# Kernel optimization log

Hardware: AMD Instinct MI355X
Metric: run time of the kernel (lower is better)

Reference implementation:

```python
import jax, jax.numpy as jnp
import numpy as np

B, T, F, H, O = 64, 4096, 100, 200, 1


def setup_inputs() -> dict:
    key = jax.random.key(0)
    ks = jax.random.split(key, 7)
    s_i = 1.0 / np.sqrt(F)
    s_h = 1.0 / np.sqrt(H)
    return {
        "x": jax.random.normal(ks[0], (B, T, F), dtype=jnp.float32),
        # input-to-hidden weights for gates [r, z, n], concatenated: [F, 3H]
        "Wi": jax.random.uniform(ks[1], (F, 3 * H), jnp.float32, -s_i, s_i),
        "bi": jnp.zeros((3 * H,), jnp.float32),
        # hidden-to-hidden weights for gates [r, z, n]: [H, 3H] (no bias for r,z in flax GRUCell)
        "Wh": jax.random.uniform(ks[2], (H, 3 * H), jnp.float32, -s_h, s_h),
        "bhn": jnp.zeros((H,), jnp.float32),  # bias only on the h->n projection
        "Wo": jax.random.uniform(ks[3], (H, O), jnp.float32, -s_h, s_h),
        "bo": jnp.zeros((O,), jnp.float32),
    }


def _gru_forward(x, Wi, bi, Wh, bhn):
    # Precompute input projections for all timesteps: [B, T, 3H]
    gi_all = jnp.einsum("btf,fg->btg", x, Wi) + bi
    gi_all = jnp.transpose(gi_all, (1, 0, 2))  # [T, B, 3H]
    h0 = jnp.zeros((x.shape[0], Wh.shape[0]), x.dtype)

    def step(h, gi):
        hh = h @ Wh  # [B, 3H]
        r = jax.nn.sigmoid(gi[:, :H] + hh[:, :H])
        z = jax.nn.sigmoid(gi[:, H:2 * H] + hh[:, H:2 * H])
        n = jnp.tanh(gi[:, 2 * H:] + r * (hh[:, 2 * H:] + bhn))
        h_new = (1.0 - z) * n + z * h  # flax GRUCell convention
        return h_new, h_new

    _, hs = jax.lax.scan(step, h0, gi_all)  # hs: [T, B, H]
    return jnp.transpose(hs, (1, 0, 2))  # [B, T, H]


def reference(x, Wi, bi, Wh, bhn, Wo, bo):
    hs = _gru_forward(x, Wi, bi, Wh, bhn)
    return jnp.einsum("bth,ho->bto", hs, Wo) + bo  # [B, T, O]
```

## Files before the change

kernel.cpp:

```cpp
#include <hip/hip_runtime.h>
#include <cstdint>

#define B_  64
#define T_  4096
#define F_  100
#define H_  200
#define G_  600

typedef _Float16 half2_t __attribute__((ext_vector_type(2)));

__device__ __forceinline__ float sigmoidf_(float x) {
    return 1.0f / (1.0f + __expf(-x));
}
__device__ __forceinline__ float tanh_fast_(float x) {
    float e = __expf(-2.0f * x);
    return (1.0f - e) / (1.0f + e);
}

__device__ __forceinline__ float fdot2_(half2_t a, half2_t b, float c) {
#if __has_builtin(__builtin_amdgcn_fdot2)
    return __builtin_amdgcn_fdot2(a, b, c, false);
#else
    return fmaf((float)a.x, (float)b.x, fmaf((float)a.y, (float)b.y, c));
#endif
}

__device__ __forceinline__ float dpp_xor1_add(float x) {
    int xi = __float_as_int(x);
    int yi = __builtin_amdgcn_update_dpp(0, xi, 0xB1, 0xF, 0xF, true);
    return x + __int_as_float(yi);
}

__global__ void prep_whp(const float* __restrict__ Wh, half2_t* __restrict__ whp) {
    int i = blockIdx.x * 256 + threadIdx.x;
    if (i < 104 * G_) {
        int k = i / G_, c = i - k * G_;
        half2_t v;
        v.x = (k < 100) ? (_Float16)Wh[(2 * k) * G_ + c] : (_Float16)0.f;
        v.y = (k < 100) ? (_Float16)Wh[(2 * k + 1) * G_ + c] : (_Float16)0.f;
        whp[i] = v;
    }
}

__global__ __launch_bounds__(640, 1)
void gi_kernel(const float* __restrict__ x, const float* __restrict__ Wi,
               const float* __restrict__ bi, float* __restrict__ gi,
               int t0, int TC) {
    __shared__ float xT[F_ * 68];
    int row0 = blockIdx.x * 64;
    int b    = row0 / TC;
    int tc0  = row0 - b * TC;
    const float* xrow = x + ((size_t)b * T_ + t0 + tc0) * F_;
    for (int i = threadIdx.x; i < 64 * F_; i += 640) {
        int r = i / F_, f = i - r * F_;
        xT[f * 68 + r] = xrow[i];
    }
    __syncthreads();
    int col = threadIdx.x < G_ ? threadIdx.x : G_ - 1;
    float acc[64];
    #pragma unroll
    for (int r = 0; r < 64; ++r) acc[r] = 0.f;
    for (int f = 0; f < F_; ++f) {
        float wi = Wi[f * G_ + col];
        const float4* xf = (const float4*)&xT[f * 68];
        #pragma unroll
        for (int q = 0; q < 16; ++q) {
            float4 v = xf[q];
            acc[4*q+0] = fmaf(v.x, wi, acc[4*q+0]);
            acc[4*q+1] = fmaf(v.y, wi, acc[4*q+1]);
            acc[4*q+2] = fmaf(v.z, wi, acc[4*q+2]);
            acc[4*q+3] = fmaf(v.w, wi, acc[4*q+3]);
        }
    }
    if (threadIdx.x < G_) {
        float bv = bi[col];
        float* grow = gi + (size_t)row0 * G_ + col;
        #pragma unroll 4
        for (int r = 0; r < 64; ++r) grow[(size_t)r * G_] = acc[r] + bv;
    }
}

__global__ __launch_bounds__(640, 1)
void scan_kernel(const float* __restrict__ gi, const half2_t* __restrict__ whp,
                 const float* __restrict__ bhn, _Float16* __restrict__ hs,
                 float* __restrict__ hstate, int TC, int first) {
    __shared__ __align__(16) _Float16 h_h[208];
    __shared__ float A_lds[G_];
    __shared__ float Hn_lds[H_];
    int b = blockIdx.x;
    int tid = threadIdx.x;
    int p = tid >> 1;
    int s = tid & 1;
    if (p >= 300) p = 299;
    int c0 = p;
    int c1 = p + 300;

    half2_t wa[52], wb[52];
    #pragma unroll
    for (int j = 0; j < 52; ++j) {
        wa[j] = whp[(52 * s + j) * G_ + c0];
        wb[j] = whp[(52 * s + j) * G_ + c1];
    }
    float bhn_r = (c1 >= 2*H_) ? bhn[c1 - 2*H_] : 0.f;

    float hj = 0.f;
    if (tid < H_) {
        hj = first ? 0.f : hstate[b * H_ + tid];
        h_h[tid] = (_Float16)hj;
    }
    if (tid >= H_ && tid < 208) h_h[tid] = (_Float16)0.f;
    __syncthreads();

    const float* girow = gi + (size_t)b * TC * G_;
    _Float16* hsb = hs + (size_t)b * TC * H_;

    float g0 = 0.f, g1 = 0.f;
    if (s == 0) { g0 = girow[c0]; g1 = girow[c1]; }
    for (int tc = 0; tc < TC; ++tc) {
        float g0n = 0.f, g1n = 0.f;
        if (s == 0 && tc + 1 < TC) {
            g0n = girow[(size_t)(tc + 1) * G_ + c0];
            g1n = girow[(size_t)(tc + 1) * G_ + c1];
        }
        float a0 = 0.f, a1 = 0.f, a2 = 0.f, a3 = 0.f;
        float b0 = 0.f, b1 = 0.f, b2 = 0.f, b3 = 0.f;
        const float4* h4 = (const float4*)(h_h + 104 * s);
        #pragma unroll
        for (int q = 0; q < 13; ++q) {
            float4 hv = h4[q];
            half2_t* hp = (half2_t*)&hv;
            a0 = fdot2_(hp[0], wa[4*q+0], a0);
            a1 = fdot2_(hp[1], wa[4*q+1], a1);
            a2 = fdot2_(hp[2], wa[4*q+2], a2);
            a3 = fdot2_(hp[3], wa[4*q+3], a3);
            b0 = fdot2_(hp[0], wb[4*q+0], b0);
            b1 = fdot2_(hp[1], wb[4*q+1], b1);
            b2 = fdot2_(hp[2], wb[4*q+2], b2);
            b3 = fdot2_(hp[3], wb[4*q+3], b3);
        }
        float accA = dpp_xor1_add((a0 + a1) + (a2 + a3));
        float accB = dpp_xor1_add((b0 + b1) + (b2 + b3));
        if (s == 0 && c0 < 300) {
            A_lds[c0] = g0 + accA;
            if (c1 < 2*H_) {
                A_lds[c1] = g1 + accB;
            } else {
                A_lds[c1] = g1;
                Hn_lds[c1 - 2*H_] = accB + bhn_r;
            }
        }
        __syncthreads();
        if (tid < H_) {
            float r = sigmoidf_(A_lds[tid]);
            float z = sigmoidf_(A_lds[H_ + tid]);
            float n = tanh_fast_(A_lds[2*H_ + tid] + r * Hn_lds[tid]);
            hj = n + z * (hj - n);
            h_h[tid] = (_Float16)hj;
            hsb[(size_t)tc * H_ + tid] = (_Float16)hj;
        }
        __syncthreads();
        g0 = g0n; g1 = g1n;
    }
    if (tid < H_) hstate[b * H_ + tid] = hj;
}

__global__ __launch_bounds__(256, 4)
void outproj_kernel(const _Float16* __restrict__ hs, const float* __restrict__ Wo,
                    const float* __restrict__ bo, float* __restrict__ out,
                    int t0, int TC) {
    int r = blockIdx.x * 256 + threadIdx.x;
    if (r >= B_ * TC) return;
    int b = r / TC, tc = r - b * TC;
    const float4* h4 = (const float4*)(hs + (size_t)r * H_);
    float acc = 0.f;
    #pragma unroll
    for (int q = 0; q < 25; ++q) {
        float4 v = h4[q];
        const _Float16* hp = (const _Float16*)&v;
        #pragma unroll
        for (int j = 0; j < 8; ++j)
            acc = fmaf((float)hp[j], Wo[q * 8 + j], acc);
    }
    out[(size_t)b * T_ + t0 + tc] = acc + bo[0];
}

extern "C" void kernel_launch(void* const* d_in, const int* in_sizes, int n_in,
                              void* d_out, int out_size, void* d_ws, size_t ws_size,
                              hipStream_t stream) {
    const float* x   = (const float*)d_in[0];
    const float* Wi  = (const float*)d_in[1];
    const float* bi  = (const float*)d_in[2];
    const float* Wh  = (const float*)d_in[3];
    const float* bhn = (const float*)d_in[4];
    const float* Wo  = (const float*)d_in[5];
    const float* bo  = (const float*)d_in[6];
    float* out = (float*)d_out;

    const size_t hstate_b = (size_t)B_ * H_ * sizeof(float);
    const size_t whp_b    = (size_t)104 * G_ * sizeof(half2_t);
    int TC = T_;
    while (TC > 64 &&
           (size_t)B_ * TC * (G_ * 4 + H_ * 2) + hstate_b + whp_b > ws_size)
        TC >>= 1;
    char* p = (char*)d_ws;
    float*    gi     = (float*)p;            p += (size_t)B_ * TC * G_ * sizeof(float);
    _Float16* hsbuf  = (_Float16*)p;         p += (size_t)B_ * TC * H_ * sizeof(_Float16);
    float*    hstate = (float*)p;            p += hstate_b;
    half2_t*  whp    = (half2_t*)p;

    prep_whp<<<dim3((104 * G_ + 255) / 256), dim3(256), 0, stream>>>(Wh, whp);

    int nchunks = T_ / TC;
    for (int c = 0; c < nchunks; ++c) {
        int t0 = c * TC;
        gi_kernel<<<dim3(B_ * TC / 64), dim3(640), 0, stream>>>(x, Wi, bi, gi, t0, TC);
        scan_kernel<<<dim3(B_), dim3(640), 0, stream>>>(gi, whp, bhn, hsbuf,
                                                        hstate, TC, c == 0);
        outproj_kernel<<<dim3((B_ * TC + 255) / 256), dim3(256), 0, stream>>>(
            hsbuf, Wo, bo, out, t0, TC);
    }
}
```

Baseline: 5.516 ms.

## Restructure GRU scan so each quad owns one hidden unit, removing a barrier

The scan kernel now assigns four lanes to each hidden unit. Those lanes split the K dimension four ways and compute the r, z and n gate dot products together, then reduce them with quad DPP shuffles. Gate activations and the state update are done in registers instead of staging through LDS, and h is double-buffered, so each timestep needs one __syncthreads instead of two. The gi buffer is interleaved per hidden unit so each quad reads its three gates contiguously. The block grows to 832 threads, and every lane in a quad evaluates the transcendentals redundantly.

```diff
diff --git a/kernel.cpp b/kernel.cpp
--- a/kernel.cpp
+++ b/kernel.cpp
@@ -6,6 +6,8 @@
 #define F_  100
 #define H_  200
 #define G_  600
+#define KP_ 224
+#define KH_ 112
 
 typedef _Float16 half2_t __attribute__((ext_vector_type(2)));
 
@@ -25,15 +27,20 @@
 #endif
 }
 
-__device__ __forceinline__ float dpp_xor1_add(float x) {
-    int xi = __float_as_int(x);
-    int yi = __builtin_amdgcn_update_dpp(0, xi, 0xB1, 0xF, 0xF, true);
-    return x + __int_as_float(yi);
+__device__ __forceinline__ float quad_sum_(float x) {
+    int y1 = __builtin_amdgcn_update_dpp(0, __float_as_int(x), 0xB1, 0xF, 0xF, true);
+    x += __int_as_float(y1);
+    int y2 = __builtin_amdgcn_update_dpp(0, __float_as_int(x), 0x4E, 0xF, 0xF, true);
+    return x + __int_as_float(y2);
+}
+__device__ __forceinline__ float quad_bcast2_(float x) {
+    int y = __builtin_amdgcn_update_dpp(0, __float_as_int(x), 0xAA, 0xF, 0xF, true);
+    return __int_as_float(y);
 }
 
 __global__ void prep_whp(const float* __restrict__ Wh, half2_t* __restrict__ whp) {
     int i = blockIdx.x * 256 + threadIdx.x;
-    if (i < 104 * G_) {
+    if (i < KH_ * G_) {
         int k = i / G_, c = i - k * G_;
         half2_t v;
         v.x = (k < 100) ? (_Float16)Wh[(2 * k) * G_ + c] : (_Float16)0.f;
@@ -73,95 +80,94 @@
         }
     }
     if (threadIdx.x < G_) {
+        int gate = col / H_;
+        int e    = col - gate * H_;
         float bv = bi[col];
-        float* grow = gi + (size_t)row0 * G_ + col;
+        float* grow = gi + (size_t)row0 * G_ + (size_t)e * 3 + gate;
         #pragma unroll 4
         for (int r = 0; r < 64; ++r) grow[(size_t)r * G_] = acc[r] + bv;
     }
 }
 
-__global__ __launch_bounds__(640, 1)
+__global__ __launch_bounds__(832, 1) __attribute__((amdgpu_waves_per_eu(4)))
 void scan_kernel(const float* __restrict__ gi, const half2_t* __restrict__ whp,
                  const float* __restrict__ bhn, _Float16* __restrict__ hs,
                  float* __restrict__ hstate, int TC, int first) {
-    __shared__ __align__(16) _Float16 h_h[208];
-    __shared__ float A_lds[G_];
-    __shared__ float Hn_lds[H_];
+    __shared__ __align__(16) _Float16 h_h[2][KP_];
     int b = blockIdx.x;
     int tid = threadIdx.x;
-    int p = tid >> 1;
-    int s = tid & 1;
-    if (p >= 300) p = 299;
-    int c0 = p;
-    int c1 = p + 300;
-
-    half2_t wa[52], wb[52];
+    int p = tid >> 2;
+    int s = tid & 3;
+    int pc = p < H_ ? p : H_ - 1;
+    bool writer = (s == 0 && p < H_);
+
+    half2_t wr[28], wz[28], wn[28];
+    const half2_t* wbase = whp + (size_t)(28 * s) * G_;
     #pragma unroll
-    for (int j = 0; j < 52; ++j) {
-        wa[j] = whp[(52 * s + j) * G_ + c0];
-        wb[j] = whp[(52 * s + j) * G_ + c1];
-    }
-    float bhn_r = (c1 >= 2*H_) ? bhn[c1 - 2*H_] : 0.f;
-
-    float hj = 0.f;
-    if (tid < H_) {
-        hj = first ? 0.f : hstate[b * H_ + tid];
-        h_h[tid] = (_Float16)hj;
-    }
-    if (tid >= H_ && tid < 208) h_h[tid] = (_Float16)0.f;
+    for (int j = 0; j < 28; ++j) {
+        wr[j] = wbase[(size_t)j * G_ + pc];
+        wz[j] = wbase[(size_t)j * G_ + H_ + pc];
+        wn[j] = wbase[(size_t)j * G_ + 2 * H_ + pc];
+    }
+    float bhn_r = (s == 2) ? bhn[pc] : 0.f;
+
+    float hj = first ? 0.f : hstate[b * H_ + pc];
+    if (writer) h_h[0][p] = (_Float16)hj;
+    if (tid < KP_ - H_) {
+        h_h[0][H_ + tid] = (_Float16)0.f;
+        h_h[1][H_ + tid] = (_Float16)0.f;
+    }
     __syncthreads();
 
     const float* girow = gi + (size_t)b * TC * G_;
     _Float16* hsb = hs + (size_t)b * TC * H_;
 
-    float g0 = 0.f, g1 = 0.f;
-    if (s == 0) { g0 = girow[c0]; g1 = girow[c1]; }
+    int p3 = pc * 3;
+    float g = (s < 3) ? girow[p3 + s] : 0.f;
+    int cur = 0;
     for (int tc = 0; tc < TC; ++tc) {
-        float g0n = 0.f, g1n = 0.f;
-        if (s == 0 && tc + 1 < TC) {
-            g0n = girow[(size_t)(tc + 1) * G_ + c0];
-            g1n = girow[(size_t)(tc + 1) * G_ + c1];
-        }
-        float a0 = 0.f, a1 = 0.f, a2 = 0.f, a3 = 0.f;
-        float b0 = 0.f, b1 = 0.f, b2 = 0.f, b3 = 0.f;
-        const float4* h4 = (const float4*)(h_h + 104 * s);
+        float gnx = (s < 3 && tc + 1 < TC)
+                  ? girow[(size_t)(tc + 1) * G_ + p3 + s] : 0.f;
+        float r0 = 0.f, r1 = 0.f, z0 = 0.f, z1 = 0.f, n0 = 0.f, n1 = 0.f;
+        const float4* h4 = (const float4*)(&h_h[cur][0]) + 7 * s;
         #pragma unroll
-        for (int q = 0; q < 13; ++q) {
+        for (int q = 0; q < 7; ++q) {
             float4 hv = h4[q];
             half2_t* hp = (half2_t*)&hv;
-            a0 = fdot2_(hp[0], wa[4*q+0], a0);
-            a1 = fdot2_(hp[1], wa[4*q+1], a1);
-            a2 = fdot2_(hp[2], wa[4*q+2], a2);
-            a3 = fdot2_(hp[3], wa[4*q+3], a3);
-            b0 = fdot2_(hp[0], wb[4*q+0], b0);
-            b1 = fdot2_(hp[1], wb[4*q+1], b1);
-            b2 = fdot2_(hp[2], wb[4*q+2], b2);
-            b3 = fdot2_(hp[3], wb[4*q+3], b3);
+            r0 = fdot2_(hp[0], wr[4*q+0], r0);
+            z0 = fdot2_(hp[0], wz[4*q+0], z0);
+            n0 = fdot2_(hp[0], wn[4*q+0], n0);
+            r1 = fdot2_(hp[1], wr[4*q+1], r1);
+            z1 = fdot2_(hp[1], wz[4*q+1], z1);
+            n1 = fdot2_(hp[1], wn[4*q+1], n1);
+            r0 = fdot2_(hp[2], wr[4*q+2], r0);
+            z0 = fdot2_(hp[2], wz[4*q+2], z0);
+            n0 = fdot2_(hp[2], wn[4*q+2], n0);
+            r1 = fdot2_(hp[3], wr[4*q+3], r1);
+            z1 = fdot2_(hp[3], wz[4*q+3], z1);
+            n1 = fdot2_(hp[3], wn[4*q+3], n1);
         }
-        float accA = dpp_xor1_add((a0 + a1) + (a2 + a3));
-        float accB = dpp_xor1_add((b0 + b1) + (b2 + b3));
-        if (s == 0 && c0 < 300) {
-            A_lds[c0] = g0 + accA;
-            if (c1 < 2*H_) {
-                A_lds[c1] = g1 + accB;
-            } else {
-                A_lds[c1] = g1;
-                Hn_lds[c1 - 2*H_] = accB + bhn_r;
-            }
+        float pr = r0 + r1, pz = z0 + z1, pn = n0 + n1;
+        pr += (s == 0) ? g : 0.f;
+        pz += (s == 1) ? g : 0.f;
+        pn += bhn_r;
+        float R = quad_sum_(pr);
+        float Z = quad_sum_(pz);
+        float N = quad_sum_(pn);
+        float gn = quad_bcast2_(g);
+        float rr = sigmoidf_(R);
+        float zz = sigmoidf_(Z);
+        float nn = tanh_fast_(gn + rr * N);
+        hj = nn + zz * (hj - nn);
+        if (writer) {
+            h_h[cur ^ 1][p] = (_Float16)hj;
+            hsb[(size_t)tc * H_ + p] = (_Float16)hj;
         }
         __syncthreads();
-        if (tid < H_) {
-            float r = sigmoidf_(A_lds[tid]);
-            float z = sigmoidf_(A_lds[H_ + tid]);
-            float n = tanh_fast_(A_lds[2*H_ + tid] + r * Hn_lds[tid]);
-            hj = n + z * (hj - n);
-            h_h[tid] = (_Float16)hj;
-            hsb[(size_t)tc * H_ + tid] = (_Float16)hj;
-        }
-        __syncthreads();
-        g0 = g0n; g1 = g1n;
-    }
-    if (tid < H_) hstate[b * H_ + tid] = hj;
+        g = gnx;
+        cur ^= 1;
+    }
+    if (writer) hstate[b * H_ + p] = hj;
 }
 
 __global__ __launch_bounds__(256, 4)
@@ -197,7 +203,7 @@
     float* out = (float*)d_out;
 
     const size_t hstate_b = (size_t)B_ * H_ * sizeof(float);
-    const size_t whp_b    = (size_t)104 * G_ * sizeof(half2_t);
+    const size_t whp_b    = (size_t)KH_ * G_ * sizeof(half2_t);
     int TC = T_;
     while (TC > 64 &&
            (size_t)B_ * TC * (G_ * 4 + H_ * 2) + hstate_b + whp_b > ws_size)
@@ -208,13 +214,13 @@
     float*    hstate = (float*)p;            p += hstate_b;
     half2_t*  whp    = (half2_t*)p;
 
-    prep_whp<<<dim3((104 * G_ + 255) / 256), dim3(256), 0, stream>>>(Wh, whp);
+    prep_whp<<<dim3((KH_ * G_ + 255) / 256), dim3(256), 0, stream>>>(Wh, whp);
 
     int nchunks = T_ / TC;
     for (int c = 0; c < nchunks; ++c) {
         int t0 = c * TC;
         gi_kernel<<<dim3(B_ * TC / 64), dim3(640), 0, stream>>>(x, Wi, bi, gi, t0, TC);
-        scan_kernel<<<dim3(B_), dim3(640), 0, stream>>>(gi, whp, bhn, hsbuf,
+        scan_kernel<<<dim3(B_), dim3(832), 0, stream>>>(gi, whp, bhn, hsbuf,
                                                         hstate, TC, c == 0);
         outproj_kernel<<<dim3((B_ * TC + 255) / 256), dim3(256), 0, stream>>>(
             hsbuf, Wo, bo, out, t0, TC);
```

After: 6.564 ms. 19.0% more time.
